# Performance work log

Measured on AMD Instinct MI355X. Metric: run time of the kernel, lower is better.

## Reference

```python
import jax, jax.numpy as jnp
import numpy as np

EPS = 1e-5

def setup_inputs() -> dict:
    key = jax.random.key(0)
    k1, k2, k3 = jax.random.split(key, 3)
    B, P, N, Cin, Cout = 16384, 32, 2, 9, 64
    pillars = jax.random.normal(k1, (B, P, N, Cin), dtype=jnp.float32)
    num_points_per_pillar = jax.random.randint(k2, (B, P), 0, N, dtype=jnp.int32)
    # nn.Linear(9, 64, bias=False): weight (out, in), kaiming-uniform-ish init
    W = jax.random.normal(k3, (Cout, Cin), dtype=jnp.float32) * (1.0 / np.sqrt(Cin))
    gamma = jnp.ones((Cout,), dtype=jnp.float32)
    beta = jnp.zeros((Cout,), dtype=jnp.float32)
    return {"pillars": pillars, "num_points_per_pillar": num_points_per_pillar,
            "W": W, "gamma": gamma, "beta": beta}

def reference(pillars, num_points_per_pillar, W, gamma, beta):
    # pillars: (B, P, N, Cin) -> linear (no bias) -> (B, P, N, Cout)
    B, P, N, _ = pillars.shape
    x = jnp.einsum('bpnc,oc->bpno', pillars, W)
    # permute(0,3,1,2): (B, Cout, P, N)
    x = jnp.transpose(x, (0, 3, 1, 2))
    C = x.shape[1]
    # BatchNorm1d(64) applied to (B*C, P*N); requires P*N == 64.
    # Training mode: batch stats over dim 0, biased variance.
    x2 = x.reshape(B * C, P * N)
    mean = jnp.mean(x2, axis=0)            # (P*N,) == (64,)
    var = jnp.mean(jnp.square(x2 - mean), axis=0)
    x2 = (x2 - mean) * jax.lax.rsqrt(var + EPS) * gamma + beta
    x = jax.nn.relu(x2).reshape(B, C, P, N)
    # max over the point dim N -> (B, C, P)
    return jnp.max(x, axis=3)
```

## Files before the change

### kernel.cpp

```cpp
#include <hip/hip_runtime.h>


#define EPS_BN 1e-5f

__global__ __launch_bounds__(64) void pfn_prep(const float* __restrict__ W,
                                               float* __restrict__ ws) {
    __shared__ float prod[64][90];
    const int o = threadIdx.x;
    float w[9];
#pragma unroll
    for (int c = 0; c < 9; ++c) w[c] = W[o * 9 + c];
#pragma unroll
    for (int c = 0; c < 9; ++c)
#pragma unroll
        for (int c2 = 0; c2 < 9; ++c2) prod[o][c * 9 + c2] = w[c] * w[c2];
#pragma unroll
    for (int c = 0; c < 9; ++c) prod[o][81 + c] = w[c];
#pragma unroll
    for (int k = 0; k < 16; ++k) ws[96 + o * 16 + k] = 0.f;
    __syncthreads();
    for (int col = o; col < 90; col += 64) {
        float s = 0.f;
        for (int r = 0; r < 64; ++r) s += prod[r][col];
        ws[col] = s;
    }
}

__global__ __launch_bounds__(256) void pfn_stats(const float* __restrict__ pillars,
                                                 const float* __restrict__ gw,
                                                 float* __restrict__ acc8,
                                                 int ntiles) {
    __shared__ float4 smP4[1152];
    __shared__ float smG[96];
    __shared__ float red[256][5];
    float* smP = (float*)smP4;

    const int tid = threadIdx.x;
    const int b_base4 = blockIdx.x * 1152;
    const float4* P4 = (const float4*)pillars;

#pragma unroll
    for (int i = tid; i < 1152; i += 256) smP4[i] = P4[b_base4 + i];
    if (tid < 90) smG[tid] = gw[tid];
    __syncthreads();

    const int lane = tid & 63;
    const int p = lane & 31;
    const int bsub = lane >> 5;
    const int b_local = (tid >> 6) * 2 + bsub;

    float v[18];
    {
        const float2* src = (const float2*)&smP[b_local * 576 + p * 18];
#pragma unroll
        for (int k = 0; k < 9; ++k) {
            const float2 t = src[k];
            v[2 * k] = t.x;
            v[2 * k + 1] = t.y;
        }
    }

    float d0 = 0.f, d1 = 0.f, q0 = 0.f, q1 = 0.f;
#pragma unroll
    for (int c = 0; c < 9; ++c) {
        const float wc = smG[81 + c];
        d0 = fmaf(wc, v[c], d0);
        d1 = fmaf(wc, v[9 + c], d1);
        float t0 = 0.f, t1 = 0.f;
#pragma unroll
        for (int c2 = 0; c2 < 9; ++c2) {
            const float g = smG[c * 9 + c2];
            t0 = fmaf(g, v[c2], t0);
            t1 = fmaf(g, v[9 + c2], t1);
        }
        q0 = fmaf(v[c], t0, q0);
        q1 = fmaf(v[9 + c], t1, q1);
    }

    red[tid][0] = d0; red[tid][1] = q0;
    red[tid][2] = d1; red[tid][3] = q1;
    __syncthreads();
    if (tid < 32) {
        float s0 = 0.f, s1 = 0.f, s2 = 0.f, s3 = 0.f;
#pragma unroll
        for (int k = 0; k < 8; ++k) {
            s0 += red[tid + 32 * k][0];
            s1 += red[tid + 32 * k][1];
            s2 += red[tid + 32 * k][2];
            s3 += red[tid + 32 * k][3];
        }
        float* acc = acc8 + (blockIdx.x & 7) * 128;
        atomicAdd(&acc[(2 * tid) * 2], s0);
        atomicAdd(&acc[(2 * tid) * 2 + 1], s1);
        atomicAdd(&acc[(2 * tid + 1) * 2], s2);
        atomicAdd(&acc[(2 * tid + 1) * 2 + 1], s3);
    }
}

__global__ __launch_bounds__(256) void pfn_main(const float* __restrict__ pillars,
                                                const float* __restrict__ W,
                                                const float* __restrict__ acc8,
                                                const float* __restrict__ gamma,
                                                const float* __restrict__ beta,
                                                float* __restrict__ out,
                                                float invBC, int ntiles) {
    __shared__ float4 smP4[1152];
    __shared__ float smW[64 * 12];
    __shared__ float smAB[128];
    float* smP = (float*)smP4;

    const int tid = threadIdx.x;
    const int b_base4 = blockIdx.x * 1152;
    const float4* P4 = (const float4*)pillars;

#pragma unroll
    for (int i = tid; i < 1152; i += 256) smP4[i] = P4[b_base4 + i];
    for (int i = tid; i < 576; i += 256) smW[(i / 9) * 12 + (i % 9)] = W[i];
    if (tid < 64) {
        const int j = tid;
        float s1 = 0.f, s2 = 0.f;
#pragma unroll
        for (int s = 0; s < 8; ++s) {
            s1 += acc8[s * 128 + j * 2];
            s2 += acc8[s * 128 + j * 2 + 1];
        }
        const float mean = s1 * invBC;
        const float var = s2 * invBC - mean * mean;
        const float a = rsqrtf(var + EPS_BN) * gamma[j];
        smAB[j] = a;
        smAB[64 + j] = beta[j] - mean * a;
    }
    __syncthreads();

    const int lane = tid & 63;
    const int p = lane & 31;
    const int bsub = lane >> 5;
    const int b_local = (tid >> 6) * 2 + bsub;
    const int b = blockIdx.x * 8 + b_local;

    float v[18];
    {
        const float2* src = (const float2*)&smP[b_local * 576 + p * 18];
#pragma unroll
        for (int k = 0; k < 9; ++k) {
            const float2 t = src[k];
            v[2 * k] = t.x;
            v[2 * k + 1] = t.y;
        }
    }
    const float a0 = smAB[2 * p], a1 = smAB[2 * p + 1];
    const float b0 = smAB[64 + 2 * p], b1 = smAB[64 + 2 * p + 1];

    float* Ob = out + (size_t)b * 2048 + p;
#pragma unroll 8
    for (int o = 0; o < 64; ++o) {
        const float4 w0 = *(const float4*)&smW[o * 12];
        const float4 w1 = *(const float4*)&smW[o * 12 + 4];
        const float wc8 = smW[o * 12 + 8];
        float x0 = 0.f, x1 = 0.f;
        x0 = fmaf(w0.x, v[0], x0); x1 = fmaf(w0.x, v[9], x1);
        x0 = fmaf(w0.y, v[1], x0); x1 = fmaf(w0.y, v[10], x1);
        x0 = fmaf(w0.z, v[2], x0); x1 = fmaf(w0.z, v[11], x1);
        x0 = fmaf(w0.w, v[3], x0); x1 = fmaf(w0.w, v[12], x1);
        x0 = fmaf(w1.x, v[4], x0); x1 = fmaf(w1.x, v[13], x1);
        x0 = fmaf(w1.y, v[5], x0); x1 = fmaf(w1.y, v[14], x1);
        x0 = fmaf(w1.z, v[6], x0); x1 = fmaf(w1.z, v[15], x1);
        x0 = fmaf(w1.w, v[7], x0); x1 = fmaf(w1.w, v[16], x1);
        x0 = fmaf(wc8, v[8], x0);  x1 = fmaf(wc8, v[17], x1);
        const float r0 = fmaxf(fmaf(x0, a0, b0), 0.f);
        const float r1 = fmaxf(fmaf(x1, a1, b1), 0.f);
        __builtin_nontemporal_store(fmaxf(r0, r1), &Ob[o * 32]);
    }
}

extern "C" void kernel_launch(void* const* d_in, const int* in_sizes, int n_in,
                              void* d_out, int out_size, void* d_ws, size_t ws_size,
                              hipStream_t stream) {
    const float* pillars = (const float*)d_in[0];
    const float* W = (const float*)d_in[2];
    const float* gamma = (const float*)d_in[3];
    const float* beta = (const float*)d_in[4];
    float* out = (float*)d_out;
    float* ws = (float*)d_ws;

    const int B = in_sizes[0] / 576;
    const int ntiles = B / 8;

    pfn_prep<<<1, 64, 0, stream>>>(W, ws);
    pfn_stats<<<ntiles, 256, 0, stream>>>(pillars, ws, ws + 96, ntiles);
    pfn_main<<<ntiles, 256, 0, stream>>>(pillars, W, ws + 96, gamma, beta, out,
                                         1.0f / ((float)B * 64.0f), ntiles);
}
```

Measured before the change: 204.9 us.

## Restructure main kernel to hold weights in registers and halve stats grid

The stats kernel now handles 16 pillars per block in two passes, with a wave-level shuffle reduction before the shared-memory reduction, which halves the block count and the number of atomics. The main kernel remaps threads so that each half-wave owns 8 output channels, keeps their 72 weights in registers, and loops over the 8 pillars in the tile. The BN scale is folded into the inputs and the shift is used as the FMA initial value, which removes per-output affine ops and repeated shared-memory weight reads. The cost is much higher register pressure in the main kernel (72 weights plus inputs), which may lower occupancy.

After: 194.2 us. -5.2%, faster.

```diff
diff --git a/kernel.cpp b/kernel.cpp
--- a/kernel.cpp
+++ b/kernel.cpp
@@ -28,66 +28,69 @@
 
 __global__ __launch_bounds__(256) void pfn_stats(const float* __restrict__ pillars,
                                                  const float* __restrict__ gw,
-                                                 float* __restrict__ acc8,
-                                                 int ntiles) {
+                                                 float* __restrict__ acc8) {
     __shared__ float4 smP4[1152];
     __shared__ float smG[96];
-    __shared__ float red[256][5];
+    __shared__ float red[4][32][5];
     float* smP = (float*)smP4;
 
     const int tid = threadIdx.x;
-    const int b_base4 = blockIdx.x * 1152;
-    const float4* P4 = (const float4*)pillars;
-
-#pragma unroll
-    for (int i = tid; i < 1152; i += 256) smP4[i] = P4[b_base4 + i];
-    if (tid < 90) smG[tid] = gw[tid];
-    __syncthreads();
-
+    const int wv = tid >> 6;
     const int lane = tid & 63;
     const int p = lane & 31;
     const int bsub = lane >> 5;
-    const int b_local = (tid >> 6) * 2 + bsub;
-
-    float v[18];
-    {
-        const float2* src = (const float2*)&smP[b_local * 576 + p * 18];
-#pragma unroll
-        for (int k = 0; k < 9; ++k) {
-            const float2 t = src[k];
-            v[2 * k] = t.x;
-            v[2 * k + 1] = t.y;
-        }
-    }
+    const int bl1 = wv * 2 + bsub;
+    const float4* P4 = (const float4*)pillars;
+
+    if (tid < 90) smG[tid] = gw[tid];
 
     float d0 = 0.f, d1 = 0.f, q0 = 0.f, q1 = 0.f;
-#pragma unroll
-    for (int c = 0; c < 9; ++c) {
-        const float wc = smG[81 + c];
-        d0 = fmaf(wc, v[c], d0);
-        d1 = fmaf(wc, v[9 + c], d1);
-        float t0 = 0.f, t1 = 0.f;
-#pragma unroll
-        for (int c2 = 0; c2 < 9; ++c2) {
-            const float g = smG[c * 9 + c2];
-            t0 = fmaf(g, v[c2], t0);
-            t1 = fmaf(g, v[9 + c2], t1);
-        }
-        q0 = fmaf(v[c], t0, q0);
-        q1 = fmaf(v[9 + c], t1, q1);
-    }
-
-    red[tid][0] = d0; red[tid][1] = q0;
-    red[tid][2] = d1; red[tid][3] = q1;
+    for (int pass = 0; pass < 2; ++pass) {
+        const int base4 = (blockIdx.x * 16 + pass * 8) * 144;
+        __syncthreads();
+#pragma unroll
+        for (int i = tid; i < 1152; i += 256) smP4[i] = P4[base4 + i];
+        __syncthreads();
+        float v[18];
+        {
+            const float2* src = (const float2*)&smP[bl1 * 576 + p * 18];
+#pragma unroll
+            for (int k = 0; k < 9; ++k) {
+                const float2 t = src[k];
+                v[2 * k] = t.x;
+                v[2 * k + 1] = t.y;
+            }
+        }
+#pragma unroll
+        for (int c = 0; c < 9; ++c) {
+            const float wc = smG[81 + c];
+            d0 = fmaf(wc, v[c], d0);
+            d1 = fmaf(wc, v[9 + c], d1);
+            float t0 = 0.f, t1 = 0.f;
+#pragma unroll
+            for (int c2 = 0; c2 < 9; ++c2) {
+                const float g = smG[c * 9 + c2];
+                t0 = fmaf(g, v[c2], t0);
+                t1 = fmaf(g, v[9 + c2], t1);
+            }
+            q0 = fmaf(v[c], t0, q0);
+            q1 = fmaf(v[9 + c], t1, q1);
+        }
+    }
+    d0 += __shfl_xor(d0, 32); q0 += __shfl_xor(q0, 32);
+    d1 += __shfl_xor(d1, 32); q1 += __shfl_xor(q1, 32);
+    __syncthreads();
+    if (lane < 32) {
+        red[wv][p][0] = d0; red[wv][p][1] = q0;
+        red[wv][p][2] = d1; red[wv][p][3] = q1;
+    }
     __syncthreads();
     if (tid < 32) {
         float s0 = 0.f, s1 = 0.f, s2 = 0.f, s3 = 0.f;
 #pragma unroll
-        for (int k = 0; k < 8; ++k) {
-            s0 += red[tid + 32 * k][0];
-            s1 += red[tid + 32 * k][1];
-            s2 += red[tid + 32 * k][2];
-            s3 += red[tid + 32 * k][3];
+        for (int w = 0; w < 4; ++w) {
+            s0 += red[w][tid][0]; s1 += red[w][tid][1];
+            s2 += red[w][tid][2]; s3 += red[w][tid][3];
         }
         float* acc = acc8 + (blockIdx.x & 7) * 128;
         atomicAdd(&acc[(2 * tid) * 2], s0);
@@ -103,73 +106,88 @@
                                                 const float* __restrict__ gamma,
                                                 const float* __restrict__ beta,
                                                 float* __restrict__ out,
-                                                float invBC, int ntiles) {
+                                                float invBC) {
     __shared__ float4 smP4[1152];
     __shared__ float smW[64 * 12];
     __shared__ float smAB[128];
     float* smP = (float*)smP4;
 
     const int tid = threadIdx.x;
-    const int b_base4 = blockIdx.x * 1152;
     const float4* P4 = (const float4*)pillars;
 
-#pragma unroll
-    for (int i = tid; i < 1152; i += 256) smP4[i] = P4[b_base4 + i];
     for (int i = tid; i < 576; i += 256) smW[(i / 9) * 12 + (i % 9)] = W[i];
+    {
+        const int base4 = blockIdx.x * 1152;
+#pragma unroll
+        for (int i = tid; i < 1152; i += 256) smP4[i] = P4[base4 + i];
+    }
     if (tid < 64) {
-        const int j = tid;
         float s1 = 0.f, s2 = 0.f;
 #pragma unroll
         for (int s = 0; s < 8; ++s) {
-            s1 += acc8[s * 128 + j * 2];
-            s2 += acc8[s * 128 + j * 2 + 1];
+            s1 += acc8[s * 128 + tid * 2];
+            s2 += acc8[s * 128 + tid * 2 + 1];
         }
         const float mean = s1 * invBC;
         const float var = s2 * invBC - mean * mean;
-        const float a = rsqrtf(var + EPS_BN) * gamma[j];
-        smAB[j] = a;
-        smAB[64 + j] = beta[j] - mean * a;
-    }
-    __syncthreads();
-
-    const int lane = tid & 63;
-    const int p = lane & 31;
-    const int bsub = lane >> 5;
-    const int b_local = (tid >> 6) * 2 + bsub;
-    const int b = blockIdx.x * 8 + b_local;
-
-    float v[18];
-    {
-        const float2* src = (const float2*)&smP[b_local * 576 + p * 18];
-#pragma unroll
-        for (int k = 0; k < 9; ++k) {
-            const float2 t = src[k];
-            v[2 * k] = t.x;
-            v[2 * k + 1] = t.y;
-        }
+        const float a = rsqrtf(var + EPS_BN) * gamma[tid];
+        smAB[tid] = a;
+        smAB[64 + tid] = beta[tid] - mean * a;
+    }
+    __syncthreads();
+
+    const int g = tid >> 5;
+    const int p = tid & 31;
+    float wr[72];
+#pragma unroll
+    for (int k = 0; k < 8; ++k) {
+        const int o = g * 8 + k;
+        const float4 wa = *(const float4*)&smW[o * 12];
+        const float4 wb = *(const float4*)&smW[o * 12 + 4];
+        wr[k * 9 + 0] = wa.x; wr[k * 9 + 1] = wa.y;
+        wr[k * 9 + 2] = wa.z; wr[k * 9 + 3] = wa.w;
+        wr[k * 9 + 4] = wb.x; wr[k * 9 + 5] = wb.y;
+        wr[k * 9 + 6] = wb.z; wr[k * 9 + 7] = wb.w;
+        wr[k * 9 + 8] = smW[o * 12 + 8];
     }
     const float a0 = smAB[2 * p], a1 = smAB[2 * p + 1];
-    const float b0 = smAB[64 + 2 * p], b1 = smAB[64 + 2 * p + 1];
-
-    float* Ob = out + (size_t)b * 2048 + p;
-#pragma unroll 8
-    for (int o = 0; o < 64; ++o) {
-        const float4 w0 = *(const float4*)&smW[o * 12];
-        const float4 w1 = *(const float4*)&smW[o * 12 + 4];
-        const float wc8 = smW[o * 12 + 8];
-        float x0 = 0.f, x1 = 0.f;
-        x0 = fmaf(w0.x, v[0], x0); x1 = fmaf(w0.x, v[9], x1);
-        x0 = fmaf(w0.y, v[1], x0); x1 = fmaf(w0.y, v[10], x1);
-        x0 = fmaf(w0.z, v[2], x0); x1 = fmaf(w0.z, v[11], x1);
-        x0 = fmaf(w0.w, v[3], x0); x1 = fmaf(w0.w, v[12], x1);
-        x0 = fmaf(w1.x, v[4], x0); x1 = fmaf(w1.x, v[13], x1);
-        x0 = fmaf(w1.y, v[5], x0); x1 = fmaf(w1.y, v[14], x1);
-        x0 = fmaf(w1.z, v[6], x0); x1 = fmaf(w1.z, v[15], x1);
-        x0 = fmaf(w1.w, v[7], x0); x1 = fmaf(w1.w, v[16], x1);
-        x0 = fmaf(wc8, v[8], x0);  x1 = fmaf(wc8, v[17], x1);
-        const float r0 = fmaxf(fmaf(x0, a0, b0), 0.f);
-        const float r1 = fmaxf(fmaf(x1, a1, b1), 0.f);
-        __builtin_nontemporal_store(fmaxf(r0, r1), &Ob[o * 32]);
+    const float bb0 = smAB[64 + 2 * p], bb1 = smAB[64 + 2 * p + 1];
+
+    float* Ob0 = out + (size_t)blockIdx.x * 16384 + g * 256 + p;
+#pragma unroll 2
+    for (int bl = 0; bl < 8; ++bl) {
+        float vs0[9], vs1[9];
+        {
+            const float2* src = (const float2*)&smP[bl * 576 + p * 18];
+#pragma unroll
+            for (int k = 0; k < 4; ++k) {
+                const float2 t = src[k];
+                vs0[2 * k] = t.x * a0;
+                vs0[2 * k + 1] = t.y * a0;
+            }
+            {
+                const float2 t = src[4];
+                vs0[8] = t.x * a0;
+                vs1[0] = t.y * a1;
+            }
+#pragma unroll
+            for (int k = 0; k < 4; ++k) {
+                const float2 t = src[5 + k];
+                vs1[1 + 2 * k] = t.x * a1;
+                vs1[2 + 2 * k] = t.y * a1;
+            }
+        }
+        float* Ob = Ob0 + bl * 2048;
+#pragma unroll
+        for (int k = 0; k < 8; ++k) {
+            float x0 = bb0, x1 = bb1;
+#pragma unroll
+            for (int c = 0; c < 9; ++c) {
+                x0 = fmaf(wr[k * 9 + c], vs0[c], x0);
+                x1 = fmaf(wr[k * 9 + c], vs1[c], x1);
+            }
+            __builtin_nontemporal_store(fmaxf(fmaxf(x0, x1), 0.f), &Ob[k * 32]);
+        }
     }
 }
 
@@ -184,10 +202,10 @@
     float* ws = (float*)d_ws;
 
     const int B = in_sizes[0] / 576;
-    const int ntiles = B / 8;
+    const float invBC = 1.0f / ((float)B * 64.0f);
 
     pfn_prep<<<1, 64, 0, stream>>>(W, ws);
-    pfn_stats<<<ntiles, 256, 0, stream>>>(pillars, ws, ws + 96, ntiles);
-    pfn_main<<<ntiles, 256, 0, stream>>>(pillars, W, ws + 96, gamma, beta, out,
-                                         1.0f / ((float)B * 64.0f), ntiles);
-}
+    pfn_stats<<<B / 16, 256, 0, stream>>>(pillars, ws, ws + 96);
+    pfn_main<<<B / 8, 256, 0, stream>>>(pillars, W, ws + 96, gamma, beta, out,
+                                        invBC);
+}
```
